# Kernel tuning notes

Measured on AMD Instinct MI355X. Metric: run time of the kernel, lower is better.

Reference implementation:

```python
import jax, jax.numpy as jnp
import numpy as np

DECAY = 0.8
CODEBOOK_SIZE = 1024
DIM = 128


def setup_inputs() -> dict:
    key = jax.random.key(0)
    k1, k2 = jax.random.split(key)
    x = jax.random.normal(k1, (16, 4096, DIM), dtype=jnp.float32)
    embed = jax.random.normal(k2, (CODEBOOK_SIZE, DIM), dtype=jnp.float32)
    ema_embed = embed * 1.0  # ema_num_initial = 1.0
    ema_num = jnp.ones((CODEBOOK_SIZE,), dtype=jnp.float32)
    return {"x": x, "embed": embed, "ema_embed": ema_embed, "ema_num": ema_num}


def reference(x, embed, ema_embed, ema_num):
    # flatten: [..., d] -> [N, d]
    shape = x.shape
    flatten = x.reshape(-1, shape[-1])  # [N, d]
    distance = -2.0 * (flatten @ embed.T) + jnp.sum(embed * embed, axis=-1)  # [N, K]
    embed_ind = jnp.argmin(distance, axis=-1)  # [N]
    quantize = embed[embed_ind.reshape(shape[:-1])]  # gather -> [..., d]

    # training branch: onehot^T @ flatten == segment_sum over code indices
    num_curr = jax.ops.segment_sum(
        jnp.ones_like(embed_ind, dtype=jnp.float32), embed_ind,
        num_segments=CODEBOOK_SIZE)  # [K]
    embed_curr = jax.ops.segment_sum(
        flatten.astype(jnp.float32), embed_ind,
        num_segments=CODEBOOK_SIZE)  # [K, d]

    ema_num_new = ema_num * DECAY + (1.0 - DECAY) * num_curr
    ema_embed_new = ema_embed * DECAY + (1.0 - DECAY) * embed_curr
    embed_new = ema_embed_new / ema_num_new[:, None]
    return quantize, embed_new, ema_embed_new, ema_num_new
```

## Files before the change

kernel.cpp:

```cpp
#include <hip/hip_runtime.h>

#define NPTS    65536
#define DIM     128
#define KCODES  1024
#define BM      128
#define TILE_C  64
#define NTHR    256
#define NTILE   (KCODES / TILE_C)

typedef _Float16 f16x8  __attribute__((ext_vector_type(8)));
typedef float    f32x16 __attribute__((ext_vector_type(16)));

__device__ __forceinline__ void gload_lds16(const void* g, void* l) {
    __builtin_amdgcn_global_load_lds(
        (const __attribute__((address_space(1))) void*)g,
        (__attribute__((address_space(3))) void*)l, 16, 0, 0);
}

__global__ __launch_bounds__(256)
void pack_kernel(const float* __restrict__ embed, _Float16* __restrict__ ebf,
                 int* __restrict__ ghist, int* __restrict__ gcursor,
                 const float* __restrict__ ema_embed, float* __restrict__ acc,
                 float* __restrict__ hn)
{
    __shared__ float partial[256];
    const int t = threadIdx.x;
    const int b = blockIdx.x;
    const int g = b * 256 + t;
    if (g < KCODES) { ghist[g] = 0; gcursor[g] = 0; }
    {
        float4 e0 = reinterpret_cast<const float4*>(ema_embed)[g];
        float4 e1 = reinterpret_cast<const float4*>(ema_embed)[g + 16384];
        reinterpret_cast<float4*>(acc)[g] =
            (float4){0.8f * e0.x, 0.8f * e0.y, 0.8f * e0.z, 0.8f * e0.w};
        reinterpret_cast<float4*>(acc)[g + 16384] =
            (float4){0.8f * e1.x, 0.8f * e1.y, 0.8f * e1.z, 0.8f * e1.w};
    }

    {
        const int tc  = g >> 10;
        const int f   = (g >> 6) & 15;
        const int l   = g & 63;
        const int nt  = f >> 3;
        const int kc  = f & 7;
        const int c   = tc * TILE_C + nt * 32 + (l & 31);
        const int d0  = kc * 16 + (l >> 5) * 8;
        const float* src = embed + (long)c * DIM + d0;
        float4 v0 = *reinterpret_cast<const float4*>(src);
        float4 v1 = *reinterpret_cast<const float4*>(src + 4);
        float vv[8] = {v0.x, v0.y, v0.z, v0.w, v1.x, v1.y, v1.z, v1.w};
        f16x8 out;
        #pragma unroll
        for (int j = 0; j < 8; ++j) out[j] = (_Float16)vv[j];
        *reinterpret_cast<f16x8*>(ebf + (long)g * 8) = out;
    }

    {
        const int c2    = b * 16 + (t >> 4);
        const int chunk = t & 15;
        const float* src = embed + (long)c2 * DIM + chunk * 8;
        float4 v0 = *reinterpret_cast<const float4*>(src);
        float4 v1 = *reinterpret_cast<const float4*>(src + 4);
        float vv[8] = {v0.x, v0.y, v0.z, v0.w, v1.x, v1.y, v1.z, v1.w};
        float ss = 0.f;
        #pragma unroll
        for (int j = 0; j < 8; ++j) {
            float r = (float)(_Float16)vv[j];
            ss += r * r;
        }
        partial[t] = ss;
        __syncthreads();
        if ((t & 15) == 0) {
            float s = 0.f;
            #pragma unroll
            for (int j = 0; j < 16; ++j) s += partial[t + j];
            hn[c2] = 0.5f * s;
        }
    }
}

__global__ __launch_bounds__(NTHR, 2)
void argmin_kernel(const float* __restrict__ x, const _Float16* __restrict__ ebf,
                   const float* __restrict__ halfnorm, const float* __restrict__ embed,
                   int* __restrict__ ind, float* __restrict__ quant,
                   int* __restrict__ ghist)
{
    __shared__ _Float16 es[2][8192];
    __shared__ int      hist[KCODES];
    __shared__ int      bidx[BM];

    const int t    = threadIdx.x;
    const int lane = t & 63;
    const int w    = t >> 6;
    const int r32  = lane & 31;
    const int ksub = lane >> 5;
    const long xbase = (long)blockIdx.x * BM * DIM;
    const int  wp    = w * 32;

    for (int i = t; i < KCODES; i += NTHR) hist[i] = 0;

    f16x8 a[8];
    {
        const long prow = xbase + (long)(wp + r32) * DIM;
        #pragma unroll
        for (int kc = 0; kc < 8; ++kc) {
            const float* s = x + prow + kc * 16 + ksub * 8;
            float4 u0 = *reinterpret_cast<const float4*>(s);
            float4 u1 = *reinterpret_cast<const float4*>(s + 4);
            float vv[8] = {u0.x, u0.y, u0.z, u0.w, u1.x, u1.y, u1.z, u1.w};
            #pragma unroll
            for (int j = 0; j < 8; ++j) a[kc][j] = (_Float16)vv[j];
        }
    }

    #pragma unroll
    for (int i = 0; i < 4; ++i) {
        const int f = w * 4 + i;
        gload_lds16(ebf + (long)f * 512 + lane * 8, &es[0][f * 512]);
    }
    float hnv_cur[2], hnv_nxt[2];
    #pragma unroll
    for (int nt = 0; nt < 2; ++nt) hnv_cur[nt] = halfnorm[nt * 32 + r32];
    __syncthreads();

    float bestv[16];
    int   besti[16];
    #pragma unroll
    for (int s = 0; s < 16; ++s) { bestv[s] = -1e30f; besti[s] = 0; }

    #pragma unroll 1
    for (int tile = 0; tile < NTILE; ++tile) {
        if (tile + 1 < NTILE) {
            const long gbase = (long)(tile + 1) * 8192;
            #pragma unroll
            for (int i = 0; i < 4; ++i) {
                const int f = w * 4 + i;
                gload_lds16(ebf + gbase + f * 512 + lane * 8, &es[(tile + 1) & 1][f * 512]);
            }
            #pragma unroll
            for (int nt = 0; nt < 2; ++nt)
                hnv_nxt[nt] = halfnorm[(tile + 1) * TILE_C + nt * 32 + r32];
        }

        #pragma unroll
        for (int nt = 0; nt < 2; ++nt) {
            f32x16 C = {0.f, 0.f, 0.f, 0.f, 0.f, 0.f, 0.f, 0.f,
                        0.f, 0.f, 0.f, 0.f, 0.f, 0.f, 0.f, 0.f};
            #pragma unroll
            for (int kc = 0; kc < 8; ++kc) {
                f16x8 B = *reinterpret_cast<const f16x8*>(
                    &es[tile & 1][(nt * 8 + kc) * 512 + lane * 8]);
                C = __builtin_amdgcn_mfma_f32_32x32x16_f16(a[kc], B, C, 0, 0, 0);
            }
            const int c = tile * TILE_C + nt * 32 + r32;
            const float hnv = hnv_cur[nt];
            #pragma unroll
            for (int reg = 0; reg < 16; ++reg) {
                float sc = C[reg] - hnv;
                if (sc > bestv[reg]) { bestv[reg] = sc; besti[reg] = c; }
            }
        }
        hnv_cur[0] = hnv_nxt[0];
        hnv_cur[1] = hnv_nxt[1];
        __syncthreads();
    }

    #pragma unroll
    for (int s = 0; s < 16; ++s) {
        float v = bestv[s];
        int   i = besti[s];
        #pragma unroll
        for (int off = 1; off < 32; off <<= 1) {
            float ov = __shfl_xor(v, off);
            int   oi = __shfl_xor(i, off);
            if (ov > v || (ov == v && oi < i)) { v = ov; i = oi; }
        }
        bestv[s] = v; besti[s] = i;
    }
    if (r32 == 0) {
        #pragma unroll
        for (int s = 0; s < 16; ++s) {
            int p = wp + (s & 3) + 8 * (s >> 2) + 4 * ksub;
            bidx[p] = besti[s];
            ind[blockIdx.x * BM + p] = besti[s];
        }
    }
    __syncthreads();

    if (t < BM) atomicAdd(&hist[bidx[t]], 1);

    float4* dst = reinterpret_cast<float4*>(quant + xbase);
    #pragma unroll
    for (int i = 0; i < 16; ++i) {
        int idx = i * NTHR + t;
        int p   = idx >> 5;
        int q   = idx & 31;
        int c   = bidx[p];
        dst[idx] = reinterpret_cast<const float4*>(embed + (long)c * DIM)[q];
    }

    __syncthreads();
    for (int i = t; i < KCODES; i += NTHR)
        if (hist[i]) atomicAdd(&ghist[i], hist[i]);
}

__global__ __launch_bounds__(256)
void scatter_kernel(const int* __restrict__ ghist, const int* __restrict__ ind,
                    const float* __restrict__ ema_num, float* __restrict__ ema_num_new,
                    int* __restrict__ gcursor, int* __restrict__ sorted,
                    int* __restrict__ scode)
{
    __shared__ int off_lds[KCODES];
    __shared__ int wsum[4];
    const int t    = threadIdx.x;
    const int lane = t & 63;
    const int w    = t >> 6;

    int v[4], pre[4];
    int s = 0;
    #pragma unroll
    for (int j = 0; j < 4; ++j) {
        v[j] = ghist[t * 4 + j];
        pre[j] = s;
        s += v[j];
    }
    int incl = s;
    #pragma unroll
    for (int off = 1; off < 64; off <<= 1) {
        int u = __shfl_up(incl, off);
        if (lane >= off) incl += u;
    }
    if (lane == 63) wsum[w] = incl;
    __syncthreads();
    if (t == 0) {
        int a = 0;
        #pragma unroll
        for (int k = 0; k < 4; ++k) { int tmp = wsum[k]; wsum[k] = a; a += tmp; }
    }
    __syncthreads();
    const int excl = wsum[w] + incl - s;
    #pragma unroll
    for (int j = 0; j < 4; ++j) off_lds[t * 4 + j] = excl + pre[j];

    if (blockIdx.x == 0) {
        #pragma unroll
        for (int j = 0; j < 4; ++j)
            ema_num_new[t * 4 + j] = ema_num[t * 4 + j] * 0.8f + 0.2f * (float)v[j];
    }
    __syncthreads();

    const int p = blockIdx.x * 256 + t;
    const int c = ind[p];
    const int pos = off_lds[c] + atomicAdd(&gcursor[c], 1);
    sorted[pos] = p;
    scode[pos]  = c;
}

__global__ __launch_bounds__(128)
void sum2_kernel(const float* __restrict__ x, const int* __restrict__ sorted,
                 const int* __restrict__ scode, float* __restrict__ acc)
{
    __shared__ int sp[64];
    __shared__ int sc[64];
    const int t = threadIdx.x;
    const int base = blockIdx.x * 64;
    if (t < 64) { sp[t] = sorted[base + t]; sc[t] = scode[base + t]; }
    __syncthreads();

    float a = 0.f;
    int cprev = sc[0];
    #pragma unroll 1
    for (int kk = 0; kk < 8; ++kk) {
        float v[8];
        #pragma unroll
        for (int i = 0; i < 8; ++i)
            v[i] = x[(long)sp[kk * 8 + i] * DIM + t];
        #pragma unroll
        for (int i = 0; i < 8; ++i) {
            const int c = sc[kk * 8 + i];
            if (c != cprev) {
                atomicAdd(&acc[(long)cprev * DIM + t], 0.2f * a);
                a = 0.f; cprev = c;
            }
            a += v[i];
        }
    }
    atomicAdd(&acc[(long)cprev * DIM + t], 0.2f * a);
}

__global__ __launch_bounds__(256)
void final_kernel(const float* __restrict__ acc, const float* __restrict__ ema_num_new,
                  float* __restrict__ embed_new)
{
    const int g = blockIdx.x * 256 + threadIdx.x;
    float4 v = reinterpret_cast<const float4*>(acc)[g];
    const float en = ema_num_new[g >> 5];
    float4 o = {v.x / en, v.y / en, v.z / en, v.w / en};
    reinterpret_cast<float4*>(embed_new)[g] = o;
}

extern "C" void kernel_launch(void* const* d_in, const int* in_sizes, int n_in,
                              void* d_out, int out_size, void* d_ws, size_t ws_size,
                              hipStream_t stream)
{
    const float* x         = (const float*)d_in[0];
    const float* embed     = (const float*)d_in[1];
    const float* ema_embed = (const float*)d_in[2];
    const float* ema_num   = (const float*)d_in[3];

    float* out0 = (float*)d_out;
    float* out1 = out0 + 8388608;
    float* out2 = out1 + 131072;
    float* out3 = out2 + 131072;

    char* ws = (char*)d_ws;
    float*    hn      = (float*)ws;
    int*      ind     = (int*)(ws + 4096);
    _Float16* ebf     = (_Float16*)(ws + 266240);
    int*      ghist   = (int*)(ws + 528384);
    int*      gcursor = (int*)(ws + 532480);
    int*      sorted  = (int*)(ws + 536576);
    int*      scode   = (int*)(ws + 798720);

    pack_kernel<<<64, 256, 0, stream>>>(embed, ebf, ghist, gcursor, ema_embed,
                                        out2, hn);
    argmin_kernel<<<NPTS / BM, NTHR, 0, stream>>>(x, ebf, hn, embed, ind, out0, ghist);
    scatter_kernel<<<NPTS / 256, 256, 0, stream>>>(ghist, ind, ema_num, out3,
                                                   gcursor, sorted, scode);
    sum2_kernel<<<NPTS / 64, 128, 0, stream>>>(x, sorted, scode, out2);
    final_kernel<<<128, 256, 0, stream>>>(out2, out3, out1);
}
```

Baseline: 97.03 us.

## Split codebook search across two blocks and merge argmin with 64-bit atomicMax

The argmin kernel now launches a 2D grid, so each block scans half of the codebook (512 codes) for its 128 points. Per-point winners are packed into a monotone 64-bit key (score bits high, inverted index low, so ties go to the lower index) and combined with a global atomicMax. A new merge kernel decodes the keys and takes over the index write, the histogram and the quantize gather. This doubles the block count to fill more CUs and raises the occupancy hint. The cost is re-reading and converting x once per half, a 64-bit atomic per point, an extra kernel launch and the kmax scratch, which aliases the sorted/scode workspace.

Result: slower. 99.65 us (+2.7%).

```diff
diff --git a/kernel.cpp b/kernel.cpp
--- a/kernel.cpp
+++ b/kernel.cpp
@@ -6,7 +6,8 @@
 #define BM      128
 #define TILE_C  64
 #define NTHR    256
-#define NTILE   (KCODES / TILE_C)
+#define HALF_C  512
+#define NTILE_H (HALF_C / TILE_C)
 
 typedef _Float16 f16x8  __attribute__((ext_vector_type(8)));
 typedef float    f32x16 __attribute__((ext_vector_type(16)));
@@ -16,12 +17,16 @@
         (const __attribute__((address_space(1))) void*)g,
         (__attribute__((address_space(3))) void*)l, 16, 0, 0);
 }
+__device__ __forceinline__ unsigned mono32(float f) {
+    unsigned u = __builtin_bit_cast(unsigned, f);
+    return (u & 0x80000000u) ? ~u : (u | 0x80000000u);
+}
 
 __global__ __launch_bounds__(256)
 void pack_kernel(const float* __restrict__ embed, _Float16* __restrict__ ebf,
                  int* __restrict__ ghist, int* __restrict__ gcursor,
                  const float* __restrict__ ema_embed, float* __restrict__ acc,
-                 float* __restrict__ hn)
+                 float* __restrict__ hn, unsigned long long* __restrict__ kmax)
 {
     __shared__ float partial[256];
     const int t = threadIdx.x;
@@ -36,6 +41,8 @@
         reinterpret_cast<float4*>(acc)[g + 16384] =
             (float4){0.8f * e1.x, 0.8f * e1.y, 0.8f * e1.z, 0.8f * e1.w};
     }
+    #pragma unroll
+    for (int k = 0; k < 4; ++k) kmax[g * 4 + k] = 0ull;
 
     {
         const int tc  = g >> 10;
@@ -79,25 +86,23 @@
     }
 }
 
-__global__ __launch_bounds__(NTHR, 2)
+__global__ __launch_bounds__(NTHR, 4)
 void argmin_kernel(const float* __restrict__ x, const _Float16* __restrict__ ebf,
-                   const float* __restrict__ halfnorm, const float* __restrict__ embed,
-                   int* __restrict__ ind, float* __restrict__ quant,
-                   int* __restrict__ ghist)
+                   const float* __restrict__ halfnorm,
+                   unsigned long long* __restrict__ kmax)
 {
     __shared__ _Float16 es[2][8192];
-    __shared__ int      hist[KCODES];
-    __shared__ int      bidx[BM];
 
     const int t    = threadIdx.x;
     const int lane = t & 63;
     const int w    = t >> 6;
     const int r32  = lane & 31;
     const int ksub = lane >> 5;
+    const int half = blockIdx.y;
     const long xbase = (long)blockIdx.x * BM * DIM;
     const int  wp    = w * 32;
-
-    for (int i = t; i < KCODES; i += NTHR) hist[i] = 0;
+    const int  cbase = half * HALF_C;
+    const _Float16* eb = ebf + (long)half * NTILE_H * 8192;
 
     f16x8 a[8];
     {
@@ -116,11 +121,11 @@
     #pragma unroll
     for (int i = 0; i < 4; ++i) {
         const int f = w * 4 + i;
-        gload_lds16(ebf + (long)f * 512 + lane * 8, &es[0][f * 512]);
+        gload_lds16(eb + (long)f * 512 + lane * 8, &es[0][f * 512]);
     }
     float hnv_cur[2], hnv_nxt[2];
     #pragma unroll
-    for (int nt = 0; nt < 2; ++nt) hnv_cur[nt] = halfnorm[nt * 32 + r32];
+    for (int nt = 0; nt < 2; ++nt) hnv_cur[nt] = halfnorm[cbase + nt * 32 + r32];
     __syncthreads();
 
     float bestv[16];
@@ -129,17 +134,17 @@
     for (int s = 0; s < 16; ++s) { bestv[s] = -1e30f; besti[s] = 0; }
 
     #pragma unroll 1
-    for (int tile = 0; tile < NTILE; ++tile) {
-        if (tile + 1 < NTILE) {
+    for (int tile = 0; tile < NTILE_H; ++tile) {
+        if (tile + 1 < NTILE_H) {
             const long gbase = (long)(tile + 1) * 8192;
             #pragma unroll
             for (int i = 0; i < 4; ++i) {
                 const int f = w * 4 + i;
-                gload_lds16(ebf + gbase + f * 512 + lane * 8, &es[(tile + 1) & 1][f * 512]);
+                gload_lds16(eb + gbase + f * 512 + lane * 8, &es[(tile + 1) & 1][f * 512]);
             }
             #pragma unroll
             for (int nt = 0; nt < 2; ++nt)
-                hnv_nxt[nt] = halfnorm[(tile + 1) * TILE_C + nt * 32 + r32];
+                hnv_nxt[nt] = halfnorm[cbase + (tile + 1) * TILE_C + nt * 32 + r32];
         }
 
         #pragma unroll
@@ -152,7 +157,7 @@
                     &es[tile & 1][(nt * 8 + kc) * 512 + lane * 8]);
                 C = __builtin_amdgcn_mfma_f32_32x32x16_f16(a[kc], B, C, 0, 0, 0);
             }
-            const int c = tile * TILE_C + nt * 32 + r32;
+            const int c = cbase + tile * TILE_C + nt * 32 + r32;
             const float hnv = hnv_cur[nt];
             #pragma unroll
             for (int reg = 0; reg < 16; ++reg) {
@@ -181,27 +186,45 @@
         #pragma unroll
         for (int s = 0; s < 16; ++s) {
             int p = wp + (s & 3) + 8 * (s >> 2) + 4 * ksub;
-            bidx[p] = besti[s];
-            ind[blockIdx.x * BM + p] = besti[s];
-        }
-    }
-    __syncthreads();
-
-    if (t < BM) atomicAdd(&hist[bidx[t]], 1);
-
-    float4* dst = reinterpret_cast<float4*>(quant + xbase);
-    #pragma unroll
-    for (int i = 0; i < 16; ++i) {
-        int idx = i * NTHR + t;
+            unsigned long long key =
+                ((unsigned long long)mono32(bestv[s]) << 32) |
+                (unsigned long long)(0x3FFu - (unsigned)besti[s]);
+            atomicMax(&kmax[blockIdx.x * BM + p], key);
+        }
+    }
+}
+
+__global__ __launch_bounds__(256)
+void merge_kernel(const unsigned long long* __restrict__ kmax,
+                  const float* __restrict__ embed, int* __restrict__ ind,
+                  float* __restrict__ quant, int* __restrict__ ghist)
+{
+    __shared__ int hist[KCODES];
+    __shared__ int bidx[256];
+    const int t    = threadIdx.x;
+    const int base = blockIdx.x * 256;
+
+    for (int i = t; i < KCODES; i += 256) hist[i] = 0;
+
+    const unsigned long long k = kmax[base + t];
+    const int best = 0x3FF - (int)(k & 0x3FFu);
+    bidx[t] = best;
+    ind[base + t] = best;
+    __syncthreads();
+    atomicAdd(&hist[best], 1);
+    __syncthreads();
+    for (int i = t; i < KCODES; i += 256)
+        if (hist[i]) atomicAdd(&ghist[i], hist[i]);
+
+    float4* dst = reinterpret_cast<float4*>(quant + (long)base * DIM);
+    #pragma unroll
+    for (int i = 0; i < 32; ++i) {
+        int idx = i * 256 + t;
         int p   = idx >> 5;
         int q   = idx & 31;
         int c   = bidx[p];
         dst[idx] = reinterpret_cast<const float4*>(embed + (long)c * DIM)[q];
     }
-
-    __syncthreads();
-    for (int i = t; i < KCODES; i += NTHR)
-        if (hist[i]) atomicAdd(&ghist[i], hist[i]);
 }
 
 __global__ __launch_bounds__(256)
@@ -314,17 +337,19 @@
     float* out3 = out2 + 131072;
 
     char* ws = (char*)d_ws;
-    float*    hn      = (float*)ws;
-    int*      ind     = (int*)(ws + 4096);
-    _Float16* ebf     = (_Float16*)(ws + 266240);
-    int*      ghist   = (int*)(ws + 528384);
-    int*      gcursor = (int*)(ws + 532480);
-    int*      sorted  = (int*)(ws + 536576);
-    int*      scode   = (int*)(ws + 798720);
+    float*              hn      = (float*)ws;
+    int*                ind     = (int*)(ws + 4096);
+    _Float16*           ebf     = (_Float16*)(ws + 266240);
+    int*                ghist   = (int*)(ws + 528384);
+    int*                gcursor = (int*)(ws + 532480);
+    unsigned long long* kmax    = (unsigned long long*)(ws + 536576);
+    int*                sorted  = (int*)(ws + 536576);
+    int*                scode   = (int*)(ws + 798720);
 
     pack_kernel<<<64, 256, 0, stream>>>(embed, ebf, ghist, gcursor, ema_embed,
-                                        out2, hn);
-    argmin_kernel<<<NPTS / BM, NTHR, 0, stream>>>(x, ebf, hn, embed, ind, out0, ghist);
+                                        out2, hn, kmax);
+    argmin_kernel<<<dim3(NPTS / BM, 2), NTHR, 0, stream>>>(x, ebf, hn, kmax);
+    merge_kernel<<<NPTS / 256, 256, 0, stream>>>(kmax, embed, ind, out0, ghist);
     scatter_kernel<<<NPTS / 256, 256, 0, stream>>>(ghist, ind, ema_num, out3,
                                                    gcursor, sorted, scode);
     sum2_kernel<<<NPTS / 64, 128, 0, stream>>>(x, sorted, scode, out2);
```
